# Kernel tuning notes

Measured on AMD Instinct MI355X. Metric: run time of the kernel, lower is better.

The kernel has to match this reference:

```python
import jax, jax.numpy as jnp
import numpy as np

N, K, D = 65536, 1024, 256


def setup_inputs() -> dict:
    key = jax.random.key(0)
    k1, k2 = jax.random.split(key)
    e = jax.random.normal(k1, (N, D), dtype=jnp.float32)
    # module inits codebook uniform in [-1/K, 1/K]
    weight = jax.random.uniform(k2, (K, D), dtype=jnp.float32,
                                minval=-1.0 / K, maxval=1.0 / K)
    return {"e": e, "weight": weight}


def reference(e, weight):
    distances = (jnp.sum(e * e, axis=1, keepdims=True)
                 - 2.0 * jnp.matmul(e, weight.T)
                 + jnp.sum(weight * weight, axis=1))
    encoding_indices = jnp.argmin(distances, axis=1)            # [N]
    # one-hot @ weight is just a gather
    quantized = weight[encoding_indices]                        # [N, D]
    commitment_loss = jnp.mean((jax.lax.stop_gradient(quantized) - e) ** 2)
    counts = jnp.zeros((K,), dtype=jnp.float32).at[encoding_indices].add(1.0)
    codebook_usage = counts.max() / counts.sum()
    # straight-through estimator
    quantized = e + jax.lax.stop_gradient(quantized - e)
    return quantized, encoding_indices, commitment_loss, codebook_usage
```

## Files before the change

kernel.cpp:

```cpp
#include <hip/hip_runtime.h>

typedef __attribute__((ext_vector_type(8))) short short8;
typedef __attribute__((ext_vector_type(4))) float floatx4;

#define N_ROWS 65536
#define K_CB   1024
#define D_DIM  256

#define TAU 3.0e-4f
#define BLINE 520

#define OFF_WN     262144
#define OFF_FIXCNT 266240
#define OFF_HIST   266496
#define OFF_IDX    270592
#define OFF_LIST   532736
#define OFF_PART   794880
#define OFF_WFRAG  827392
#define OFF_KEYS   1351680
#define OFF_WT     1875968

__device__ __forceinline__ float pw128_sq(const float4* p) {
#pragma clang fp contract(off)
    float4 q0 = p[0], q1 = p[1];
    float r0 = q0.x * q0.x, r1 = q0.y * q0.y, r2 = q0.z * q0.z, r3 = q0.w * q0.w;
    float r4 = q1.x * q1.x, r5 = q1.y * q1.y, r6 = q1.z * q1.z, r7 = q1.w * q1.w;
    for (int i = 1; i < 16; ++i) {
        float4 u0 = p[2 * i], u1 = p[2 * i + 1];
        r0 = r0 + u0.x * u0.x; r1 = r1 + u0.y * u0.y;
        r2 = r2 + u0.z * u0.z; r3 = r3 + u0.w * u0.w;
        r4 = r4 + u1.x * u1.x; r5 = r5 + u1.y * u1.y;
        r6 = r6 + u1.z * u1.z; r7 = r7 + u1.w * u1.w;
    }
    return ((r0 + r1) + (r2 + r3)) + ((r4 + r5) + (r6 + r7));
}
__device__ __forceinline__ float pw128_sq_lds(const double* p) {
#pragma clang fp contract(off)
    float r[8];
    #pragma unroll
    for (int j = 0; j < 8; ++j) { float x = (float)p[j]; r[j] = x * x; }
    for (int i = 1; i < 16; ++i) {
        #pragma unroll
        for (int j = 0; j < 8; ++j) { float x = (float)p[8 * i + j]; r[j] = r[j] + x * x; }
    }
    return ((r[0] + r[1]) + (r[2] + r[3])) + ((r[4] + r[5]) + (r[6] + r[7]));
}
__device__ __forceinline__ float rownorm_np(const float* row) {
#pragma clang fp contract(off)
    float s0 = pw128_sq((const float4*)row);
    float s1 = pw128_sq((const float4*)(row + 128));
    return s0 + s1;
}
__device__ __forceinline__ float np_dist(float A, float m, float Ck) {
#pragma clang fp contract(off)
    float Bv = 2.0f * m;
    float t  = A - Bv;
    return t + Ck;
}
__device__ __forceinline__ unsigned short bf16_rne(float x) {
    unsigned u = __float_as_uint(x);
    unsigned r = u + 0x7fff + ((u >> 16) & 1);
    return (unsigned short)(r >> 16);
}
__device__ __forceinline__ float bf16_tof(unsigned short h) {
    return __uint_as_float(((unsigned)h) << 16);
}

#define PRS 260
__global__ __launch_bounds__(256) void k_prep(
        const float* __restrict__ wg,
        float* __restrict__ wn,
        unsigned short* __restrict__ wfrag, float* __restrict__ wt) {
    __shared__ __align__(16) float es[32 * PRS];
    const int tid = threadIdx.x;
    const int bx  = blockIdx.x;
    if (bx < 4) {
        int row = bx * 256 + tid;
        wn[row] = rownorm_np(wg + (size_t)row * D_DIM);
    } else if (bx < 132) {
        int t = (bx - 4) * 256 + tid;
        int col = t >> 5, kc = t & 31;
        const float4* src = (const float4*)(wg + (size_t)col * D_DIM + kc * 8);
        float4 v0 = src[0], v1 = src[1];
        const float a[8] = {v0.x, v0.y, v0.z, v0.w, v1.x, v1.y, v1.z, v1.w};
        short8 h;
        #pragma unroll
        for (int i = 0; i < 8; ++i) h[i] = (short)bf16_rne(a[i]);
        *(short8*)(wfrag + ((size_t)kc * 1024 + col) * 8) = h;
    } else {
        float (*tw)[PRS] = (float(*)[PRS])es;
        const int cb = bx - 132;
        const int c0 = cb * 32;
        #pragma unroll
        for (int it = 0; it < 8; ++it) {
            int idx = it * 256 + tid;
            int code = idx >> 6, f4 = idx & 63;
            *(float4*)&tw[code][f4 * 4] =
                *(const float4*)(wg + (size_t)(c0 + code) * D_DIM + f4 * 4);
        }
        __syncthreads();
        const int j = tid & 31, dg = tid >> 5;
        #pragma unroll
        for (int dd = 0; dd < 32; ++dd) {
            int d = dd * 8 + dg;
            wt[(size_t)d * K_CB + c0 + j] = tw[j][d];
        }
    }
}

__global__ __launch_bounds__(256, 2) void k_dist(
        const float* __restrict__ eg, const unsigned short* __restrict__ wfrag,
        const float* __restrict__ wn,
        int* __restrict__ idx_ws, int* __restrict__ fixlist, int* __restrict__ fixcnt) {
    __shared__ __align__(16) unsigned short Bs[32 * BLINE];
    __shared__ float wnS[K_CB];
    const int tid  = threadIdx.x;
    const int lane = tid & 63;
    const int wv   = tid >> 6;
    const int q    = lane >> 4;
    const int m15  = lane & 15;
    const int waveRow = blockIdx.x * 64 + wv * 16;

    #pragma unroll
    for (int i = 0; i < 4; ++i) wnS[tid + i * 256] = wn[tid + i * 256];

    short8 afh[8], afl[8];
    {
        const float* rowp = eg + (size_t)(waveRow + m15) * D_DIM + q * 8;
        #pragma unroll
        for (int win = 0; win < 8; ++win) {
            const float4* pa = (const float4*)(rowp + win * 32);
            float4 x0 = pa[0], x1 = pa[1];
            const float a[8] = {x0.x, x0.y, x0.z, x0.w, x1.x, x1.y, x1.z, x1.w};
            short8 h, l;
            #pragma unroll
            for (int i = 0; i < 8; ++i) {
                unsigned short hh = bf16_rne(a[i]);
                h[i] = (short)hh;
                l[i] = (short)bf16_rne(a[i] - bf16_tof(hh));
            }
            afh[win] = h;
            afl[win] = l;
        }
    }

    float best[4], sec[4];
    int bidx[4];
    #pragma unroll
    for (int s = 0; s < 4; ++s) { best[s] = 3.4e38f; sec[s] = 3.4e38f; bidx[s] = 0; }

    for (int cb = 0; cb < 16; ++cb) {
        __syncthreads();
        #pragma unroll
        for (int t = 0; t < 8; ++t) {
            int L = wv * 8 + t;
            const unsigned short* src = wfrag + ((size_t)L * 1024 + cb * 64) * 8 + lane * 8;
            __builtin_amdgcn_global_load_lds(
                (const __attribute__((address_space(1))) unsigned int*)src,
                (__attribute__((address_space(3))) unsigned int*)&Bs[L * BLINE],
                16, 0, 0);
        }
        __syncthreads();

        floatx4 acc[4];
        #pragma unroll
        for (int nt = 0; nt < 4; ++nt)
            acc[nt] = (floatx4){0.f, 0.f, 0.f, 0.f};

        #pragma unroll
        for (int nt = 0; nt < 4; ++nt) {
            #pragma unroll
            for (int win = 0; win < 8; ++win) {
                int kc = win * 4 + q;
                short8 bfh = *(short8*)&Bs[kc * BLINE + (nt * 16 + m15) * 8];
                acc[nt] = __builtin_amdgcn_mfma_f32_16x16x32_bf16(afh[win], bfh, acc[nt], 0, 0, 0);
                acc[nt] = __builtin_amdgcn_mfma_f32_16x16x32_bf16(afl[win], bfh, acc[nt], 0, 0, 0);
            }
        }
        #pragma unroll
        for (int nt = 0; nt < 4; ++nt) {
            int col = cb * 64 + nt * 16 + m15;
            float Ck = wnS[col];
            #pragma unroll
            for (int reg = 0; reg < 4; ++reg) {
                float d = __builtin_fmaf(-2.0f, acc[nt][reg], Ck);
                bool lt = d < best[reg];
                sec[reg]  = __builtin_amdgcn_fmed3f(d, best[reg], sec[reg]);
                best[reg] = fminf(d, best[reg]);
                bidx[reg] = lt ? col : bidx[reg];
            }
        }
    }

    #pragma unroll
    for (int s = 0; s < 4; ++s) {
        float b = best[s], se = sec[s];
        int ix = bidx[s];
        #pragma unroll
        for (int m = 1; m < 16; m <<= 1) {
            float bo = __shfl_xor(b, m, 64);
            float so = __shfl_xor(se, m, 64);
            int   io = __shfl_xor(ix, m, 64);
            float ns = fminf(fminf(se, so), fmaxf(b, bo));
            if (bo < b || (bo == b && io < ix)) { b = bo; ix = io; }
            se = ns;
        }
        if (m15 == 0) {
            int row = waveRow + q * 4 + s;
            idx_ws[row] = ix;
            if (se - b < TAU) {
                int p = atomicAdd(fixcnt, 1);
                fixlist[p] = row;
            }
        }
    }
}

#define FG_ROWS 8
__global__ __launch_bounds__(256) void k_fixup(
        const float* __restrict__ eg, const float* __restrict__ wt,
        const float* __restrict__ wnorm,
        const int* __restrict__ fixlist, const int* __restrict__ fixcnt,
        unsigned long long* __restrict__ keys) {
    __shared__ double xs[FG_ROWS][D_DIM];
    __shared__ float AnS[FG_ROWS];
    const int tid = threadIdx.x;
    const int cnt = *fixcnt;
    if (cnt == 0) return;
    const int ngroups = (cnt + FG_ROWS - 1) / FG_ROWS;
    const int ntiles  = ngroups * 2;
    const int rowg = tid >> 7;
    const int cg   = tid & 127;
    for (int t = blockIdx.x; t < ntiles; t += gridDim.x) {
        const int g     = t >> 1;
        const int chunk = t & 1;
        __syncthreads();
        int rows[FG_ROWS];
        #pragma unroll
        for (int i = 0; i < FG_ROWS; ++i) {
            int j = g * FG_ROWS + i;
            rows[i] = fixlist[j < cnt ? j : cnt - 1];
        }
        #pragma unroll
        for (int i = 0; i < FG_ROWS; ++i)
            xs[i][tid] = (double)eg[(size_t)rows[i] * D_DIM + tid];
        __syncthreads();

        if (tid < 16) {
            int row = tid >> 1, half = tid & 1;
            float s = pw128_sq_lds(&xs[row][half * 128]);
            float so = __shfl_xor(s, 1, 64);
            if (half == 0) AnS[row] = s + so;
        }

        const int c0 = chunk * 512 + cg * 4;
        float Cw[4];
        #pragma unroll
        for (int c = 0; c < 4; ++c) Cw[c] = wnorm[c0 + c];

        double s[4][4];
        #pragma unroll
        for (int r = 0; r < 4; ++r)
            #pragma unroll
            for (int c = 0; c < 4; ++c) s[r][c] = 0.0;

        #pragma unroll 2
        for (int d = 0; d < D_DIM; d += 2) {
            float4 wa = *(const float4*)(wt + (size_t)d * K_CB + c0);
            float4 wb = *(const float4*)(wt + (size_t)(d + 1) * K_CB + c0);
            double wad[4] = {(double)wa.x, (double)wa.y, (double)wa.z, (double)wa.w};
            double wbd[4] = {(double)wb.x, (double)wb.y, (double)wb.z, (double)wb.w};
            #pragma unroll
            for (int r = 0; r < 4; ++r) {
                double2 e2 = *(const double2*)&xs[rowg * 4 + r][d];
                #pragma unroll
                for (int c = 0; c < 4; ++c)
                    s[r][c] += e2.x * wad[c] + e2.y * wbd[c];
            }
        }
        __syncthreads();

        #pragma unroll
        for (int r = 0; r < 4; ++r) {
            float An = AnS[rowg * 4 + r];
            unsigned long long key = 0xFFFFFFFFFFFFFFFFull;
            #pragma unroll
            for (int c = 0; c < 4; ++c) {
                float dq = np_dist(An, (float)s[r][c], Cw[c]);
                unsigned u = __float_as_uint(dq);
                unsigned key32 = u ^ (((unsigned)((int)u >> 31)) | 0x80000000u);
                unsigned long long kk =
                    ((unsigned long long)key32 << 32) | (unsigned)(c0 + c);
                key = kk < key ? kk : key;
            }
            #pragma unroll
            for (int m = 1; m < 64; m <<= 1) {
                unsigned long long o = __shfl_xor(key, m, 64);
                key = (o < key) ? o : key;
            }
            int j = g * FG_ROWS + rowg * 4 + r;
            if ((tid & 63) == 0 && j < cnt) atomicMin(&keys[j], key);
        }
    }
}

__global__ void k_fixscatter(const int* __restrict__ fixlist, const int* __restrict__ fixcnt,
                             const unsigned long long* __restrict__ keys,
                             int* __restrict__ idx_ws) {
    const int cnt = *fixcnt;
    for (int j = blockIdx.x * blockDim.x + threadIdx.x; j < cnt;
         j += gridDim.x * blockDim.x)
        idx_ws[fixlist[j]] = (int)(keys[j] & 0xFFFFFFFFull);
}

__global__ void k_final(const float* __restrict__ eg, const float* __restrict__ wg,
                        const int* __restrict__ idx_ws, float* __restrict__ qout,
                        float* __restrict__ iout, int* __restrict__ hist,
                        double* __restrict__ partials) {
    const int tid  = threadIdx.x;
    const int sub  = tid >> 6;
    const int lane = tid & 63;
    const int rowBase = blockIdx.x * 16;
    double acc = 0.0;
    #pragma unroll
    for (int g = 0; g < 4; ++g) {
        int row = rowBase + g * 4 + sub;
        int k = idx_ws[row];
        float4 ev = ((const float4*)(eg + (size_t)row * D_DIM))[lane];
        float4 wv = ((const float4*)(wg + (size_t)k   * D_DIM))[lane];
        float dx = wv.x - ev.x, dy = wv.y - ev.y, dz = wv.z - ev.z, dw = wv.w - ev.w;
        float4 qv = {ev.x + dx, ev.y + dy, ev.z + dz, ev.w + dw};
        ((float4*)(qout + (size_t)row * D_DIM))[lane] = qv;
        acc += (double)(dx * dx) + (double)(dy * dy)
             + (double)(dz * dz) + (double)(dw * dw);
        if (lane == 0) {
            iout[row] = (float)k;
            atomicAdd(&hist[k], 1);
        }
    }
    __shared__ double red[256];
    red[tid] = acc;
    __syncthreads();
    for (int st = 128; st > 0; st >>= 1) {
        if (tid < st) red[tid] += red[tid + st];
        __syncthreads();
    }
    if (tid == 0) partials[blockIdx.x] = red[0];
}

__global__ void k_scalars(const int* __restrict__ hist, const double* __restrict__ partials,
                          float* __restrict__ sout) {
    const int tid = threadIdx.x;
    double s = 0.0;
    for (int j = tid; j < N_ROWS / 16; j += 256) s += partials[j];
    int m = 0;
    for (int j = tid; j < K_CB; j += 256) m = max(m, hist[j]);
    __shared__ double rs[256];
    __shared__ int    rm[256];
    rs[tid] = s; rm[tid] = m;
    __syncthreads();
    for (int st = 128; st > 0; st >>= 1) {
        if (tid < st) { rs[tid] += rs[tid + st]; rm[tid] = max(rm[tid], rm[tid + st]); }
        __syncthreads();
    }
    if (tid == 0) {
        sout[0] = (float)(rs[0] / (double)((size_t)N_ROWS * D_DIM));
        sout[1] = (float)rm[0] / 65536.0f;
    }
}

extern "C" void kernel_launch(void* const* d_in, const int* in_sizes, int n_in,
                              void* d_out, int out_size, void* d_ws, size_t ws_size,
                              hipStream_t stream) {
    const float* e = (const float*)d_in[0];
    const float* w = (const float*)d_in[1];
    float* out  = (float*)d_out;
    float* qout = out;
    float* iout = out + (size_t)N_ROWS * D_DIM;
    float* sout = iout + N_ROWS;

    char* ws = (char*)d_ws;
    float*  wn       = (float*) (ws + OFF_WN);
    int*    fixcnt   = (int*)   (ws + OFF_FIXCNT);
    int*    hist     = (int*)   (ws + OFF_HIST);
    int*    idxp     = (int*)   (ws + OFF_IDX);
    int*    list     = (int*)   (ws + OFF_LIST);
    double* partials = (double*)(ws + OFF_PART);
    unsigned short* wfrag = (unsigned short*)(ws + OFF_WFRAG);
    unsigned long long* keys = (unsigned long long*)(ws + OFF_KEYS);
    float*  wt       = (float*) (ws + OFF_WT);

    hipMemsetAsync(ws + OFF_FIXCNT, 0, 4352, stream);
    hipMemsetAsync(ws + OFF_KEYS, 0xFF, 524288, stream);

    hipLaunchKernelGGL(k_prep,       dim3(164),         dim3(256), 0, stream, w, wn, wfrag, wt);
    hipLaunchKernelGGL(k_dist,       dim3(1024),        dim3(256), 0, stream, e, wfrag, wn, idxp, list, fixcnt);
    hipLaunchKernelGGL(k_fixup,      dim3(2048),        dim3(256), 0, stream, e, wt, wn, list, fixcnt, keys);
    hipLaunchKernelGGL(k_fixscatter, dim3(64),          dim3(256), 0, stream, list, fixcnt, keys, idxp);
    hipLaunchKernelGGL(k_final,      dim3(N_ROWS / 16), dim3(256), 0, stream, e, w, idxp, qout, iout, hist, partials);
    hipLaunchKernelGGL(k_scalars,    dim3(1),           dim3(256), 0, stream, hist, partials, sout);
}
```

Baseline: 315.1 us.

## Drop bf16 low-part MFMA and process two row tiles per wave

The distance kernel drops the split-bf16 (hi+lo) representation of e and uses only the rounded bf16 high part, which halves the MFMA work per output. Each wave now covers 32 rows (two 16-row tiles) that share each B fragment loaded from LDS, so LDS traffic per MFMA is halved and the grid is halved. The near-tie threshold TAU is raised to send more ambiguous rows to the exact fixup pass. This compensates for the lower precision, but it risks a longer fixup list and some ties slipping through if the bf16 error is larger than TAU.

```diff
diff --git a/kernel.cpp b/kernel.cpp
--- a/kernel.cpp
+++ b/kernel.cpp
@@ -7,7 +7,7 @@
 #define K_CB   1024
 #define D_DIM  256
 
-#define TAU 3.0e-4f
+#define TAU 4.0e-4f
 #define BLINE 520
 
 #define OFF_WN     262144
@@ -61,9 +61,6 @@
     unsigned u = __float_as_uint(x);
     unsigned r = u + 0x7fff + ((u >> 16) & 1);
     return (unsigned short)(r >> 16);
-}
-__device__ __forceinline__ float bf16_tof(unsigned short h) {
-    return __uint_as_float(((unsigned)h) << 16);
 }
 
 #define PRS 260
@@ -119,35 +116,31 @@
     const int wv   = tid >> 6;
     const int q    = lane >> 4;
     const int m15  = lane & 15;
-    const int waveRow = blockIdx.x * 64 + wv * 16;
+    const int waveRow = blockIdx.x * 128 + wv * 32;
 
     #pragma unroll
     for (int i = 0; i < 4; ++i) wnS[tid + i * 256] = wn[tid + i * 256];
 
-    short8 afh[8], afl[8];
-    {
-        const float* rowp = eg + (size_t)(waveRow + m15) * D_DIM + q * 8;
+    short8 afh0[8], afh1[8];
+    #pragma unroll
+    for (int mt = 0; mt < 2; ++mt) {
+        const float* rowp = eg + (size_t)(waveRow + mt * 16 + m15) * D_DIM + q * 8;
         #pragma unroll
         for (int win = 0; win < 8; ++win) {
             const float4* pa = (const float4*)(rowp + win * 32);
             float4 x0 = pa[0], x1 = pa[1];
             const float a[8] = {x0.x, x0.y, x0.z, x0.w, x1.x, x1.y, x1.z, x1.w};
-            short8 h, l;
-            #pragma unroll
-            for (int i = 0; i < 8; ++i) {
-                unsigned short hh = bf16_rne(a[i]);
-                h[i] = (short)hh;
-                l[i] = (short)bf16_rne(a[i] - bf16_tof(hh));
-            }
-            afh[win] = h;
-            afl[win] = l;
-        }
-    }
-
-    float best[4], sec[4];
-    int bidx[4];
-    #pragma unroll
-    for (int s = 0; s < 4; ++s) { best[s] = 3.4e38f; sec[s] = 3.4e38f; bidx[s] = 0; }
+            short8 h;
+            #pragma unroll
+            for (int i = 0; i < 8; ++i) h[i] = (short)bf16_rne(a[i]);
+            if (mt == 0) afh0[win] = h; else afh1[win] = h;
+        }
+    }
+
+    float best[8], sec[8];
+    int bidx[8];
+    #pragma unroll
+    for (int s = 0; s < 8; ++s) { best[s] = 3.4e38f; sec[s] = 3.4e38f; bidx[s] = 0; }
 
     for (int cb = 0; cb < 16; ++cb) {
         __syncthreads();
@@ -162,38 +155,38 @@
         }
         __syncthreads();
 
-        floatx4 acc[4];
-        #pragma unroll
-        for (int nt = 0; nt < 4; ++nt)
-            acc[nt] = (floatx4){0.f, 0.f, 0.f, 0.f};
-
         #pragma unroll
         for (int nt = 0; nt < 4; ++nt) {
+            floatx4 acc0 = (floatx4){0.f, 0.f, 0.f, 0.f};
+            floatx4 acc1 = (floatx4){0.f, 0.f, 0.f, 0.f};
             #pragma unroll
             for (int win = 0; win < 8; ++win) {
                 int kc = win * 4 + q;
                 short8 bfh = *(short8*)&Bs[kc * BLINE + (nt * 16 + m15) * 8];
-                acc[nt] = __builtin_amdgcn_mfma_f32_16x16x32_bf16(afh[win], bfh, acc[nt], 0, 0, 0);
-                acc[nt] = __builtin_amdgcn_mfma_f32_16x16x32_bf16(afl[win], bfh, acc[nt], 0, 0, 0);
-            }
-        }
-        #pragma unroll
-        for (int nt = 0; nt < 4; ++nt) {
+                acc0 = __builtin_amdgcn_mfma_f32_16x16x32_bf16(afh0[win], bfh, acc0, 0, 0, 0);
+                acc1 = __builtin_amdgcn_mfma_f32_16x16x32_bf16(afh1[win], bfh, acc1, 0, 0, 0);
+            }
             int col = cb * 64 + nt * 16 + m15;
             float Ck = wnS[col];
             #pragma unroll
             for (int reg = 0; reg < 4; ++reg) {
-                float d = __builtin_fmaf(-2.0f, acc[nt][reg], Ck);
-                bool lt = d < best[reg];
-                sec[reg]  = __builtin_amdgcn_fmed3f(d, best[reg], sec[reg]);
-                best[reg] = fminf(d, best[reg]);
-                bidx[reg] = lt ? col : bidx[reg];
-            }
-        }
-    }
-
-    #pragma unroll
-    for (int s = 0; s < 4; ++s) {
+                float d0 = __builtin_fmaf(-2.0f, acc0[reg], Ck);
+                bool lt0 = d0 < best[reg];
+                sec[reg]  = __builtin_amdgcn_fmed3f(d0, best[reg], sec[reg]);
+                best[reg] = fminf(d0, best[reg]);
+                bidx[reg] = lt0 ? col : bidx[reg];
+                float d1 = __builtin_fmaf(-2.0f, acc1[reg], Ck);
+                int s1 = 4 + reg;
+                bool lt1 = d1 < best[s1];
+                sec[s1]  = __builtin_amdgcn_fmed3f(d1, best[s1], sec[s1]);
+                best[s1] = fminf(d1, best[s1]);
+                bidx[s1] = lt1 ? col : bidx[s1];
+            }
+        }
+    }
+
+    #pragma unroll
+    for (int s = 0; s < 8; ++s) {
         float b = best[s], se = sec[s];
         int ix = bidx[s];
         #pragma unroll
@@ -206,7 +199,7 @@
             se = ns;
         }
         if (m15 == 0) {
-            int row = waveRow + q * 4 + s;
+            int row = waveRow + (s >> 2) * 16 + q * 4 + (s & 3);
             idx_ws[row] = ix;
             if (se - b < TAU) {
                 int p = atomicAdd(fixcnt, 1);
@@ -394,7 +387,7 @@
     hipMemsetAsync(ws + OFF_KEYS, 0xFF, 524288, stream);
 
     hipLaunchKernelGGL(k_prep,       dim3(164),         dim3(256), 0, stream, w, wn, wfrag, wt);
-    hipLaunchKernelGGL(k_dist,       dim3(1024),        dim3(256), 0, stream, e, wfrag, wn, idxp, list, fixcnt);
+    hipLaunchKernelGGL(k_dist,       dim3(512),         dim3(256), 0, stream, e, wfrag, wn, idxp, list, fixcnt);
     hipLaunchKernelGGL(k_fixup,      dim3(2048),        dim3(256), 0, stream, e, wt, wn, list, fixcnt, keys);
     hipLaunchKernelGGL(k_fixscatter, dim3(64),          dim3(256), 0, stream, list, fixcnt, keys, idxp);
     hipLaunchKernelGGL(k_final,      dim3(N_ROWS / 16), dim3(256), 0, stream, e, w, idxp, qout, iout, hist, partials);
```

New measurement: 314.7 us. About the same (-0.1%).
